# Kernel optimization log

Measured on AMD Instinct MI355X. Metric: run time of the kernel, lower is better.

Reference implementation:

```python
import jax, jax.numpy as jnp
import numpy as np

HEADS = 8
DQK = 64
DV = 64
SPAN = 32
STRIDE = 1


def setup_inputs() -> dict:
    key = jax.random.key(0)
    ks = jax.random.split(key, 7)
    B, Lq, Lkv = 2, 4096, 4096
    dq = dk = dv = 512
    dout = 512
    w_scale = 0.02
    return {
        "q": jax.random.normal(ks[0], (B, Lq, dq), jnp.float32),
        "k": jax.random.normal(ks[1], (B, Lkv, dk), jnp.float32),
        "v": jax.random.normal(ks[2], (B, Lkv, dv), jnp.float32),
        "Wq": jax.random.normal(ks[3], (dq, HEADS * DQK), jnp.float32) * w_scale,
        "Wk": jax.random.normal(ks[4], (dk, HEADS * DQK), jnp.float32) * w_scale,
        "Wv": jax.random.normal(ks[5], (dv, HEADS * DV), jnp.float32) * w_scale,
        "Wo": jax.random.normal(ks[6], (HEADS * DV, dout), jnp.float32) * w_scale,
    }


def reference(q, k, v, Wq, Wk, Wv, Wo):
    B, Lq, _ = q.shape
    Lkv = k.shape[1]
    # projections -> [B, H, L, d]
    Q = (q @ Wq).reshape(B, Lq, HEADS, DQK).transpose(0, 2, 1, 3)
    K = (k @ Wk).reshape(B, Lkv, HEADS, DQK).transpose(0, 2, 1, 3)
    V = (v @ Wv).reshape(B, Lkv, HEADS, DV).transpose(0, 2, 1, 3)

    # sliding window indices: kvi[r, j] = r - (span-1) + stride*j  -> [span, Lq]
    r = jnp.arange(SPAN)
    j = jnp.arange(Lq)
    kvi = r[:, None] - (SPAN - 1) + STRIDE * j[None, :]
    valid = (kvi >= 0) & (kvi < Lkv)                      # [span, Lq]
    kvs = jnp.clip(kvi, 0, Lkv - 1)

    Kg = K[:, :, kvs, :]                                   # [B, H, span, Lq, dQK]
    scores = jnp.einsum("bhjd,bhrjd->bhrj", Q, Kg) / (DQK ** 0.5)
    scores = jnp.where(valid, scores, -jnp.inf)
    # faithful to original: softmax over dim=3 == length_q axis
    W = jax.nn.softmax(scores, axis=3)                     # [B, H, span, Lq]
    W = jnp.where(valid, W, 0.0)

    Vg = V[:, :, kvs, :]                                   # [B, H, span, Lq, dV]
    O = jnp.einsum("bhrj,bhrjd->bhjd", W, Vg)              # sum over span
    out = O.transpose(0, 2, 1, 3).reshape(B, Lq, HEADS * DV) @ Wo
    return out
```

## Files before the change

kernel.cpp:

```cpp
#include <hip/hip_runtime.h>
#include <hip/hip_bf16.h>

#define L_Q 4096
#define NB 2
#define DMODEL 512
#define NHEAD 8
#define DHEAD 64
#define SPAN_ 32

using short8 = __attribute__((ext_vector_type(8))) short;
using f32x4  = __attribute__((ext_vector_type(4))) float;

typedef __attribute__((address_space(1))) const void GV;
typedef __attribute__((address_space(3))) void LV;

__device__ __forceinline__ void gl2lds16(const void* g, void* l) {
    __builtin_amdgcn_global_load_lds((GV*)g, (LV*)l, 16, 0, 0);
}

__device__ __forceinline__ float bf2f(short u) {
    return __uint_as_float(((unsigned)(unsigned short)u) << 16);
}
__device__ __forceinline__ short f2bf(float f) {
    __hip_bfloat16 h = __float2bfloat16(f);
    return *reinterpret_cast<short*>(&h);
}
__device__ __forceinline__ unsigned packbf(float lo, float hi) {
    return (unsigned)(unsigned short)f2bf(lo) | ((unsigned)(unsigned short)f2bf(hi) << 16);
}

__global__ __launch_bounds__(256) void castT4_bf16(
    const float* __restrict__ Wq, const float* __restrict__ Wk,
    const float* __restrict__ Wv, const float* __restrict__ Wo,
    short* __restrict__ Wtq, short* __restrict__ Wtk,
    short* __restrict__ Wtv, short* __restrict__ Wto)
{
    const int z = blockIdx.z;
    const float* W = (z == 0) ? Wq : ((z == 1) ? Wk : ((z == 2) ? Wv : Wo));
    short* Wt = (z == 0) ? Wtq : ((z == 1) ? Wtk : ((z == 2) ? Wtv : Wto));
    __shared__ float t[32][33];
    const int tx = threadIdx.x, ty = threadIdx.y;
    const int bx = blockIdx.x, by = blockIdx.y;
#pragma unroll
    for (int i = 0; i < 4; ++i)
        t[ty + i * 8][tx] = W[(size_t)(by * 32 + ty + i * 8) * DMODEL + bx * 32 + tx];
    __syncthreads();
#pragma unroll
    for (int i = 0; i < 4; ++i)
        Wt[(size_t)(bx * 32 + ty + i * 8) * DMODEL + by * 32 + tx] = f2bf(t[tx][ty + i * 8]);
}

__device__ __forceinline__ void xcd_swizzle(int& m0, int& n0) {
    int hw = blockIdx.x + (blockIdx.y << 2);
    int xcd = hw & 7, slot = hw >> 3;
    int mt = xcd * 8 + (slot >> 2);
    int nt = slot & 3;
    m0 = mt * 128;
    n0 = nt * 128;
}

template<int OUTMODE, bool AF32>
__device__ __forceinline__ void gemm128_body(
    const void* __restrict__ Avoid, const short* __restrict__ Bt, void* __restrict__ Cout,
    void* AsRaw, short* Bs, int m0, int n0)
{
    const int tid = threadIdx.x;
    const int w = tid >> 6, lane = tid & 63;
    const int wr = w & 1, wc = w >> 1;
    const int l15 = lane & 15, l4 = lane >> 4;
    float* Asf = (float*)AsRaw;
    short* Asb = (short*)AsRaw;

    f32x4 acc[4][4];
#pragma unroll
    for (int fm = 0; fm < 4; ++fm)
#pragma unroll
        for (int fn = 0; fn < 4; ++fn) acc[fm][fn] = (f32x4){0.f, 0.f, 0.f, 0.f};

    for (int k0 = 0; k0 < DMODEL; k0 += 64) {
        __syncthreads();
        if (AF32) {
            const float* Af = (const float*)Avoid;
#pragma unroll
            for (int it = 0; it < 8; ++it) {
                int c = it * 256 + tid;
                int row = c >> 4, slot = c & 15;
                gl2lds16(Af + (size_t)(m0 + row) * DMODEL + k0 + ((slot ^ (row & 15)) << 2),
                         &Asf[c * 4]);
            }
        } else {
            const short* Ab = (const short*)Avoid;
#pragma unroll
            for (int it = 0; it < 4; ++it) {
                int c = it * 256 + tid;
                int row = c >> 3, slot = c & 7;
                gl2lds16(Ab + (size_t)(m0 + row) * DMODEL + k0 + ((slot ^ (row & 7)) << 3),
                         &Asb[c * 8]);
            }
        }
#pragma unroll
        for (int it = 0; it < 4; ++it) {
            int c = it * 256 + tid;
            int row = c >> 3, slot = c & 7;
            gl2lds16(Bt + (size_t)(n0 + row) * DMODEL + k0 + ((slot ^ (row & 7)) << 3), &Bs[c * 8]);
        }
        __syncthreads();
#pragma unroll
        for (int ks = 0; ks < 2; ++ks) {
            const int koff = ks * 4 + l4;
            short8 a[4], b[4];
#pragma unroll
            for (int fm = 0; fm < 4; ++fm) {
                int row = wr * 64 + fm * 16 + l15;
                if (AF32) {
                    int rx = row & 15;
                    float4 f0 = *(const float4*)&Asf[row * 64 + (((koff * 2)     ^ rx) << 2)];
                    float4 f1 = *(const float4*)&Asf[row * 64 + (((koff * 2 + 1) ^ rx) << 2)];
                    short8 o;
                    o[0] = f2bf(f0.x); o[1] = f2bf(f0.y); o[2] = f2bf(f0.z); o[3] = f2bf(f0.w);
                    o[4] = f2bf(f1.x); o[5] = f2bf(f1.y); o[6] = f2bf(f1.z); o[7] = f2bf(f1.w);
                    a[fm] = o;
                } else {
                    a[fm] = *(const short8*)&Asb[(row * 8 + (koff ^ (row & 7))) * 8];
                }
            }
#pragma unroll
            for (int fn = 0; fn < 4; ++fn) {
                int row = wc * 64 + fn * 16 + l15;
                b[fn] = *(const short8*)&Bs[(row * 8 + (koff ^ (row & 7))) * 8];
            }
#pragma unroll
            for (int fm = 0; fm < 4; ++fm)
#pragma unroll
                for (int fn = 0; fn < 4; ++fn)
                    acc[fm][fn] = __builtin_amdgcn_mfma_f32_16x16x32_bf16(
                        a[fm], b[fn], acc[fm][fn], 0, 0, 0);
        }
    }
#pragma unroll
    for (int fm = 0; fm < 4; ++fm)
#pragma unroll
        for (int fn = 0; fn < 4; ++fn) {
            if (OUTMODE == 2) {
                short4 o4;
                o4.x = f2bf(acc[fm][fn][0]);
                o4.y = f2bf(acc[fm][fn][1]);
                o4.z = f2bf(acc[fm][fn][2]);
                o4.w = f2bf(acc[fm][fn][3]);
                int m = m0 + wr * 64 + fm * 16 + l4 * 4;
                int bb = m >> 12, g = m & (L_Q - 1);
                int n = n0 + wc * 64 + fn * 16 + l15;
                int hh = n >> 6, dd = n & 63;
                *(short4*)&((short*)Cout)[(((size_t)bb * NHEAD + hh) * DHEAD + dd) * L_Q + g] = o4;
            } else {
#pragma unroll
                for (int i = 0; i < 4; ++i) {
                    size_t row = (size_t)(m0 + wr * 64 + fm * 16 + l4 * 4 + i);
                    int col = n0 + wc * 64 + fn * 16 + l15;
                    if (OUTMODE == 1) ((short*)Cout)[row * DMODEL + col] = f2bf(acc[fm][fn][i]);
                    else              ((float*)Cout)[row * DMODEL + col] = acc[fm][fn][i];
                }
            }
        }
}

__global__ __launch_bounds__(256) void gemm_qkv(
    const float* __restrict__ q, const float* __restrict__ k, const float* __restrict__ v,
    const short* __restrict__ Wtq, const short* __restrict__ Wtk, const short* __restrict__ Wtv,
    short* __restrict__ Qp, short* __restrict__ Kp, short* __restrict__ Vt)
{
    __shared__ float Asf[128 * 64];
    __shared__ short Bs[128 * 64];
    int m0, n0;
    xcd_swizzle(m0, n0);
    const int z = blockIdx.z;
    const float* A  = (z == 0) ? q   : ((z == 1) ? k   : v);
    const short* Bt = (z == 0) ? Wtq : ((z == 1) ? Wtk : Wtv);
    if (z == 2) gemm128_body<2, true>(A, Bt, Vt, Asf, Bs, m0, n0);
    else        gemm128_body<1, true>(A, Bt, (z == 0) ? Qp : Kp, Asf, Bs, m0, n0);
}

__global__ __launch_bounds__(256) void gemm_fin(
    const short* __restrict__ Op, const short* __restrict__ Wto, float* __restrict__ out)
{
    __shared__ short As[128 * 64];
    __shared__ short Bs[128 * 64];
    int m0, n0;
    xcd_swizzle(m0, n0);
    gemm128_body<0, false>(Op, Wto, out, As, Bs, m0, n0);
}

__global__ __launch_bounds__(256) void attn_e(
    const short* __restrict__ Qp, const short* __restrict__ Kp,
    float* __restrict__ part)
{
    __shared__ short Ks[160 * 64];
    __shared__ short Qs[128 * 64];
    __shared__ float eb[128][36];
    __shared__ float red[8][32];
    const int tid = threadIdx.x;
    const int j0 = blockIdx.x * 128;
    const int h = blockIdx.y, b = blockIdx.z;
    const int bh = b * NHEAD + h;
    const int w = tid >> 6, lane = tid & 63;
    const int l15 = lane & 15, l4 = lane >> 4;

    {
        float4 z = make_float4(0.f, 0.f, 0.f, 0.f);
        float4* ebv = (float4*)&eb[0][0];
#pragma unroll
        for (int i = 0; i < 5; ++i) {
            int idx = i * 256 + tid;
            if (idx < 1152) ebv[idx] = z;
        }
    }
#pragma unroll
    for (int it = 0; it < 5; ++it) {
        int c = it * 256 + tid;
        int row = c >> 3, slot = c & 7;
        int g = j0 - 31 + row;
        g = (g < 0) ? 0 : ((g > L_Q - 1) ? L_Q - 1 : g);
        gl2lds16(Kp + ((size_t)b * L_Q + g) * DMODEL + h * DHEAD + ((slot ^ (row & 7)) << 3), &Ks[c * 8]);
    }
#pragma unroll
    for (int it = 0; it < 4; ++it) {
        int c = it * 256 + tid;
        int row = c >> 3, slot = c & 7;
        gl2lds16(Qp + ((size_t)b * L_Q + j0 + row) * DMODEL + h * DHEAD + ((slot ^ (row & 7)) << 3), &Qs[c * 8]);
    }
    __syncthreads();

    f32x4 acc[2][4];
#pragma unroll
    for (int tm = 0; tm < 2; ++tm)
#pragma unroll
        for (int tn = 0; tn < 4; ++tn) acc[tm][tn] = (f32x4){0.f, 0.f, 0.f, 0.f};
#pragma unroll
    for (int kk = 0; kk < 2; ++kk) {
        const int koff = kk * 4 + l4;
        short8 af[2], bf[4];
#pragma unroll
        for (int tm = 0; tm < 2; ++tm) {
            int row = w * 32 + tm * 16 + l15;
            af[tm] = *(const short8*)&Qs[(row * 8 + (koff ^ (row & 7))) * 8];
        }
#pragma unroll
        for (int tn = 0; tn < 4; ++tn) {
            int row = w * 32 + tn * 16 + l15;
            bf[tn] = *(const short8*)&Ks[(row * 8 + (koff ^ (row & 7))) * 8];
        }
#pragma unroll
        for (int tm = 0; tm < 2; ++tm)
#pragma unroll
            for (int tn = 0; tn < 4; ++tn)
                acc[tm][tn] = __builtin_amdgcn_mfma_f32_16x16x32_bf16(
                    af[tm], bf[tn], acc[tm][tn], 0, 0, 0);
    }

    const int gbase = j0 + w * 32 - 31;
#pragma unroll
    for (int tm = 0; tm < 2; ++tm)
#pragma unroll
        for (int tn = 0; tn < 4; ++tn)
#pragma unroll
            for (int i = 0; i < 4; ++i) {
                int q = tm * 16 + l4 * 4 + i;
                int rr = tn * 16 + l15;
                int r = rr - q;
                bool valid = (r >= 0) && (r < SPAN_) && (gbase + rr >= 0);
                if (valid) eb[w * 32 + q][r] = __expf(acc[tm][tn][i] * 0.125f);
            }
    __syncthreads();

    {
        int r = tid & 31, grp = tid >> 5;
        float s = 0.f;
#pragma unroll
        for (int qq = 0; qq < 16; ++qq) s += eb[grp * 16 + qq][r];
        red[grp][r] = s;
    }
    __syncthreads();
    if (tid < 32) {
        float s = 0.f;
#pragma unroll
        for (int g = 0; g < 8; ++g) s += red[g][tid];
        part[((size_t)bh * SPAN_ + tid) * 32 + blockIdx.x] = s;
    }
}

__global__ __launch_bounds__(256) void attn_o(
    const short* __restrict__ Qp, const short* __restrict__ Kp,
    const short* __restrict__ Vt, const float* __restrict__ part,
    short* __restrict__ Op)
{
    __shared__ short Ks[160 * 64];
    __shared__ short Qs[128 * 64];
    __shared__ short Vts[64 * 192];
    const int tid = threadIdx.x;
    const int j0 = blockIdx.x * 128;
    const int h = blockIdx.y, b = blockIdx.z;
    const int bh = b * NHEAD + h;
    const int w = tid >> 6, lane = tid & 63;
    const int l15 = lane & 15, l4 = lane >> 4;

#pragma unroll
    for (int it = 0; it < 5; ++it) {
        int c = it * 256 + tid;
        int row = c >> 3, slot = c & 7;
        int g = j0 - 32 + row;
        g = (g < 0) ? 0 : ((g > L_Q - 1) ? L_Q - 1 : g);
        gl2lds16(Kp + ((size_t)b * L_Q + g) * DMODEL + h * DHEAD + ((slot ^ (row & 7)) << 3), &Ks[c * 8]);
    }
#pragma unroll
    for (int it = 0; it < 4; ++it) {
        int c = it * 256 + tid;
        int row = c >> 3, slot = c & 7;
        gl2lds16(Qp + ((size_t)b * L_Q + j0 + row) * DMODEL + h * DHEAD + ((slot ^ (row & 7)) << 3), &Qs[c * 8]);
    }
#pragma unroll
    for (int it = 0; it < 6; ++it) {
        int c = it * 256 + tid;
        int d = c / 24, cs = c - d * 24;
        int gg = j0 - 32 + ((cs ^ (d & 7)) << 3);
        gg = (gg < 0) ? 0 : ((gg > L_Q - 8) ? L_Q - 8 : gg);
        gl2lds16(Vt + ((size_t)bh * DHEAD + d) * L_Q + gg, &Vts[c * 8]);
    }

    float iv;
    {
        const float4* pp = (const float4*)(part + ((size_t)bh * SPAN_ + (lane & 31)) * 32);
        float s = 0.f;
#pragma unroll
        for (int i = 0; i < 8; ++i) {
            float4 t = pp[i];
            s += t.x + t.y + t.z + t.w;
        }
        iv = 1.0f / s;
    }
    __syncthreads();

    f32x4 sa[4][2];
#pragma unroll
    for (int tk = 0; tk < 4; ++tk)
#pragma unroll
        for (int tq = 0; tq < 2; ++tq) sa[tk][tq] = (f32x4){0.f, 0.f, 0.f, 0.f};
#pragma unroll
    for (int kk = 0; kk < 2; ++kk) {
        const int koff = kk * 4 + l4;
        short8 af[4], qf[2];
#pragma unroll
        for (int tk = 0; tk < 4; ++tk) {
            int row = w * 32 + tk * 16 + l15;
            af[tk] = *(const short8*)&Ks[(row * 8 + (koff ^ (row & 7))) * 8];
        }
#pragma unroll
        for (int tq = 0; tq < 2; ++tq) {
            int row = w * 32 + tq * 16 + l15;
            qf[tq] = *(const short8*)&Qs[(row * 8 + (koff ^ (row & 7))) * 8];
        }
#pragma unroll
        for (int tk = 0; tk < 4; ++tk)
#pragma unroll
            for (int tq = 0; tq < 2; ++tq)
                sa[tk][tq] = __builtin_amdgcn_mfma_f32_16x16x32_bf16(
                    af[tk], qf[tq], sa[tk][tq], 0, 0, 0);
    }

    const int gbase = j0 + w * 32 - 32;
#pragma unroll
    for (int tk = 0; tk < 4; ++tk)
#pragma unroll
        for (int tq = 0; tq < 2; ++tq)
#pragma unroll
            for (int i = 0; i < 4; ++i) {
                int rrp = tk * 16 + l4 * 4 + i;
                int q = tq * 16 + l15;
                int r = rrp - q - 1;
                bool valid = (r >= 0) && (r < SPAN_) && (gbase + rrp >= 0);
                float e = __expf(sa[tk][tq][i] * 0.125f) * __shfl(iv, r & 31);
                sa[tk][tq][i] = valid ? e : 0.f;
            }

    unsigned pk[4][2][2];
#pragma unroll
    for (int tk = 0; tk < 4; ++tk)
#pragma unroll
        for (int tq = 0; tq < 2; ++tq) {
            pk[tk][tq][0] = packbf(sa[tk][tq][0], sa[tk][tq][1]);
            pk[tk][tq][1] = packbf(sa[tk][tq][2], sa[tk][tq][3]);
        }

    const int hi = l4 >> 1;
    const int lsA = ((l4 & 1) << 5) + l15;

    f32x4 oa[2][4];
#pragma unroll
    for (int tm = 0; tm < 2; ++tm)
#pragma unroll
        for (int dn = 0; dn < 4; ++dn) oa[tm][dn] = (f32x4){0.f, 0.f, 0.f, 0.f};
#pragma unroll
    for (int kk = 0; kk < 2; ++kk) {
        short8 pa[2];
#pragma unroll
        for (int tm = 0; tm < 2; ++tm) {
            unsigned lo00 = (unsigned)__shfl((int)pk[kk * 2 + 0][tm][0], lsA);
            unsigned hi00 = (unsigned)__shfl((int)pk[kk * 2 + 1][tm][0], lsA);
            unsigned lo01 = (unsigned)__shfl((int)pk[kk * 2 + 0][tm][1], lsA);
            unsigned hi01 = (unsigned)__shfl((int)pk[kk * 2 + 1][tm][1], lsA);
            unsigned lo10 = (unsigned)__shfl((int)pk[kk * 2 + 0][tm][0], lsA + 16);
            unsigned hi10 = (unsigned)__shfl((int)pk[kk * 2 + 1][tm][0], lsA + 16);
            unsigned lo11 = (unsigned)__shfl((int)pk[kk * 2 + 0][tm][1], lsA + 16);
            unsigned hi11 = (unsigned)__shfl((int)pk[kk * 2 + 1][tm][1], lsA + 16);
            uint4 wds;
            wds.x = hi ? hi00 : lo00;
            wds.y = hi ? hi01 : lo01;
            wds.z = hi ? hi10 : lo10;
            wds.w = hi ? hi11 : lo11;
            pa[tm] = *reinterpret_cast<short8*>(&wds);
        }
#pragma unroll
        for (int dn = 0; dn < 4; ++dn) {
            int row = dn * 16 + l15;
            int cs = w * 4 + kk * 4 + l4;
            short8 vb = *(const short8*)&Vts[row * 192 + ((cs ^ (row & 7)) << 3)];
#pragma unroll
            for (int tm = 0; tm < 2; ++tm)
                oa[tm][dn] = __builtin_amdgcn_mfma_f32_16x16x32_bf16(
                    pa[tm], vb, oa[tm][dn], 0, 0, 0);
        }
    }

#pragma unroll
    for (int tm = 0; tm < 2; ++tm)
#pragma unroll
        for (int dn = 0; dn < 4; ++dn)
#pragma unroll
            for (int i = 0; i < 4; ++i) {
                int q = w * 32 + tm * 16 + l4 * 4 + i;
                Op[((size_t)b * L_Q + j0 + q) * DMODEL + h * DHEAD + dn * 16 + l15] =
                    f2bf(oa[tm][dn][i]);
            }
}

extern "C" void kernel_launch(void* const* d_in, const int* in_sizes, int n_in,
                              void* d_out, int out_size, void* d_ws, size_t ws_size,
                              hipStream_t stream) {
    (void)in_sizes; (void)n_in; (void)out_size; (void)ws_size;
    const float* q  = (const float*)d_in[0];
    const float* k  = (const float*)d_in[1];
    const float* v  = (const float*)d_in[2];
    const float* Wq = (const float*)d_in[3];
    const float* Wk = (const float*)d_in[4];
    const float* Wv = (const float*)d_in[5];
    const float* Wo = (const float*)d_in[6];
    float* out = (float*)d_out;

    char* ws = (char*)d_ws;
    const size_t MiB = 1ull << 20;
    short* Wtq = (short*)(ws);
    short* Wtk = (short*)(ws + 512 * 1024);
    short* Wtv = (short*)(ws + 1 * MiB);
    short* Wto = (short*)(ws + 1 * MiB + 512 * 1024);
    short* Qp  = (short*)(ws + 2 * MiB);
    short* Kp  = (short*)(ws + 10 * MiB);
    short* Vtp = (short*)(ws + 18 * MiB);
    short* Op  = (short*)(ws + 26 * MiB);
    float* part = (float*)(ws + 34 * MiB);

    castT4_bf16<<<dim3(16, 16, 4), dim3(32, 8), 0, stream>>>(
        Wq, Wk, Wv, Wo, Wtq, Wtk, Wtv, Wto);

    gemm_qkv<<<dim3(4, 64, 3), 256, 0, stream>>>(q, k, v, Wtq, Wtk, Wtv, Qp, Kp, Vtp);

    dim3 ga(L_Q / 128, NHEAD, NB);
    attn_e<<<ga, 256, 0, stream>>>(Qp, Kp, part);
    attn_o<<<ga, 256, 0, stream>>>(Qp, Kp, Vtp, part, Op);

    gemm_fin<<<dim3(4, 64), 256, 0, stream>>>(Op, Wto, out);
}
```

Before: 64.18 us.

## Double-buffer GEMM LDS tiles and merge QKV projections into one persistent loop

The two projection GEMMs now double-buffer their LDS tiles, prefetching the next K-slice with global_load_lds while MFMAs run on the current one, with a single barrier per step. The QKV kernel no longer launches a z-dimension; each block loops over all three projections in sequence (24 stages), writing each output after 8 stages and resetting its accumulators. The aim is to hide global load latency and cut barriers. In exchange the QKV grid shrinks to 256 blocks, and QKV LDS use doubles to about 96KB, which can lower occupancy.

```diff
diff --git a/kernel.cpp b/kernel.cpp
--- a/kernel.cpp
+++ b/kernel.cpp
@@ -59,135 +59,193 @@
     n0 = nt * 128;
 }
 
-template<int OUTMODE, bool AF32>
-__device__ __forceinline__ void gemm128_body(
-    const void* __restrict__ Avoid, const short* __restrict__ Bt, void* __restrict__ Cout,
-    void* AsRaw, short* Bs, int m0, int n0)
-{
-    const int tid = threadIdx.x;
-    const int w = tid >> 6, lane = tid & 63;
-    const int wr = w & 1, wc = w >> 1;
-    const int l15 = lane & 15, l4 = lane >> 4;
-    float* Asf = (float*)AsRaw;
-    short* Asb = (short*)AsRaw;
-
-    f32x4 acc[4][4];
-#pragma unroll
-    for (int fm = 0; fm < 4; ++fm)
-#pragma unroll
-        for (int fn = 0; fn < 4; ++fn) acc[fm][fn] = (f32x4){0.f, 0.f, 0.f, 0.f};
-
-    for (int k0 = 0; k0 < DMODEL; k0 += 64) {
-        __syncthreads();
-        if (AF32) {
-            const float* Af = (const float*)Avoid;
-#pragma unroll
-            for (int it = 0; it < 8; ++it) {
-                int c = it * 256 + tid;
-                int row = c >> 4, slot = c & 15;
-                gl2lds16(Af + (size_t)(m0 + row) * DMODEL + k0 + ((slot ^ (row & 15)) << 2),
-                         &Asf[c * 4]);
-            }
-        } else {
-            const short* Ab = (const short*)Avoid;
-#pragma unroll
-            for (int it = 0; it < 4; ++it) {
-                int c = it * 256 + tid;
-                int row = c >> 3, slot = c & 7;
-                gl2lds16(Ab + (size_t)(m0 + row) * DMODEL + k0 + ((slot ^ (row & 7)) << 3),
-                         &Asb[c * 8]);
-            }
-        }
-#pragma unroll
-        for (int it = 0; it < 4; ++it) {
-            int c = it * 256 + tid;
-            int row = c >> 3, slot = c & 7;
-            gl2lds16(Bt + (size_t)(n0 + row) * DMODEL + k0 + ((slot ^ (row & 7)) << 3), &Bs[c * 8]);
-        }
-        __syncthreads();
-#pragma unroll
-        for (int ks = 0; ks < 2; ++ks) {
-            const int koff = ks * 4 + l4;
-            short8 a[4], b[4];
-#pragma unroll
-            for (int fm = 0; fm < 4; ++fm) {
-                int row = wr * 64 + fm * 16 + l15;
-                if (AF32) {
-                    int rx = row & 15;
-                    float4 f0 = *(const float4*)&Asf[row * 64 + (((koff * 2)     ^ rx) << 2)];
-                    float4 f1 = *(const float4*)&Asf[row * 64 + (((koff * 2 + 1) ^ rx) << 2)];
-                    short8 o;
-                    o[0] = f2bf(f0.x); o[1] = f2bf(f0.y); o[2] = f2bf(f0.z); o[3] = f2bf(f0.w);
-                    o[4] = f2bf(f1.x); o[5] = f2bf(f1.y); o[6] = f2bf(f1.z); o[7] = f2bf(f1.w);
-                    a[fm] = o;
-                } else {
-                    a[fm] = *(const short8*)&Asb[(row * 8 + (koff ^ (row & 7))) * 8];
-                }
-            }
-#pragma unroll
-            for (int fn = 0; fn < 4; ++fn) {
-                int row = wc * 64 + fn * 16 + l15;
-                b[fn] = *(const short8*)&Bs[(row * 8 + (koff ^ (row & 7))) * 8];
-            }
-#pragma unroll
-            for (int fm = 0; fm < 4; ++fm)
-#pragma unroll
-                for (int fn = 0; fn < 4; ++fn)
-                    acc[fm][fn] = __builtin_amdgcn_mfma_f32_16x16x32_bf16(
-                        a[fm], b[fn], acc[fm][fn], 0, 0, 0);
-        }
-    }
-#pragma unroll
-    for (int fm = 0; fm < 4; ++fm)
-#pragma unroll
-        for (int fn = 0; fn < 4; ++fn) {
-            if (OUTMODE == 2) {
-                short4 o4;
-                o4.x = f2bf(acc[fm][fn][0]);
-                o4.y = f2bf(acc[fm][fn][1]);
-                o4.z = f2bf(acc[fm][fn][2]);
-                o4.w = f2bf(acc[fm][fn][3]);
-                int m = m0 + wr * 64 + fm * 16 + l4 * 4;
-                int bb = m >> 12, g = m & (L_Q - 1);
-                int n = n0 + wc * 64 + fn * 16 + l15;
-                int hh = n >> 6, dd = n & 63;
-                *(short4*)&((short*)Cout)[(((size_t)bb * NHEAD + hh) * DHEAD + dd) * L_Q + g] = o4;
-            } else {
-#pragma unroll
-                for (int i = 0; i < 4; ++i) {
-                    size_t row = (size_t)(m0 + wr * 64 + fm * 16 + l4 * 4 + i);
-                    int col = n0 + wc * 64 + fn * 16 + l15;
-                    if (OUTMODE == 1) ((short*)Cout)[row * DMODEL + col] = f2bf(acc[fm][fn][i]);
-                    else              ((float*)Cout)[row * DMODEL + col] = acc[fm][fn][i];
-                }
-            }
-        }
-}
-
 __global__ __launch_bounds__(256) void gemm_qkv(
     const float* __restrict__ q, const float* __restrict__ k, const float* __restrict__ v,
     const short* __restrict__ Wtq, const short* __restrict__ Wtk, const short* __restrict__ Wtv,
     short* __restrict__ Qp, short* __restrict__ Kp, short* __restrict__ Vt)
 {
-    __shared__ float Asf[128 * 64];
-    __shared__ short Bs[128 * 64];
+    __shared__ float AsF[2][128 * 64];
+    __shared__ short Bs[2][128 * 64];
     int m0, n0;
     xcd_swizzle(m0, n0);
-    const int z = blockIdx.z;
-    const float* A  = (z == 0) ? q   : ((z == 1) ? k   : v);
-    const short* Bt = (z == 0) ? Wtq : ((z == 1) ? Wtk : Wtv);
-    if (z == 2) gemm128_body<2, true>(A, Bt, Vt, Asf, Bs, m0, n0);
-    else        gemm128_body<1, true>(A, Bt, (z == 0) ? Qp : Kp, Asf, Bs, m0, n0);
+    const int tid = threadIdx.x;
+    const int w = tid >> 6, lane = tid & 63;
+    const int wr = w & 1, wc = w >> 1;
+    const int l15 = lane & 15, l4 = lane >> 4;
+
+    auto stage = [&](int idx, int buf) {
+        const int z = idx >> 3;
+        const int k0 = (idx & 7) << 6;
+        const float* Af = (z == 0) ? q : ((z == 1) ? k : v);
+        const short* Bt = (z == 0) ? Wtq : ((z == 1) ? Wtk : Wtv);
+#pragma unroll
+        for (int it = 0; it < 8; ++it) {
+            int c = it * 256 + tid;
+            int row = c >> 4, slot = c & 15;
+            gl2lds16(Af + (size_t)(m0 + row) * DMODEL + k0 + ((slot ^ (row & 15)) << 2),
+                     &AsF[buf][c * 4]);
+        }
+#pragma unroll
+        for (int it = 0; it < 4; ++it) {
+            int c = it * 256 + tid;
+            int row = c >> 3, slot = c & 7;
+            gl2lds16(Bt + (size_t)(n0 + row) * DMODEL + k0 + ((slot ^ (row & 7)) << 3),
+                     &Bs[buf][c * 8]);
+        }
+    };
+
+    f32x4 acc[4][4];
+#pragma unroll
+    for (int fm = 0; fm < 4; ++fm)
+#pragma unroll
+        for (int fn = 0; fn < 4; ++fn) acc[fm][fn] = (f32x4){0.f, 0.f, 0.f, 0.f};
+
+    stage(0, 0);
+    __syncthreads();
+    int cur = 0;
+
+    for (int idx = 0; idx < 24; ++idx) {
+        if (idx < 23) stage(idx + 1, cur ^ 1);
+
+#pragma unroll
+        for (int ks = 0; ks < 2; ++ks) {
+            const int koff = ks * 4 + l4;
+            short8 a[4], b[4];
+#pragma unroll
+            for (int fm = 0; fm < 4; ++fm) {
+                int row = wr * 64 + fm * 16 + l15;
+                int rx = row & 15;
+                float4 f0 = *(const float4*)&AsF[cur][row * 64 + (((koff * 2)     ^ rx) << 2)];
+                float4 f1 = *(const float4*)&AsF[cur][row * 64 + (((koff * 2 + 1) ^ rx) << 2)];
+                short8 o;
+                o[0] = f2bf(f0.x); o[1] = f2bf(f0.y); o[2] = f2bf(f0.z); o[3] = f2bf(f0.w);
+                o[4] = f2bf(f1.x); o[5] = f2bf(f1.y); o[6] = f2bf(f1.z); o[7] = f2bf(f1.w);
+                a[fm] = o;
+            }
+#pragma unroll
+            for (int fn = 0; fn < 4; ++fn) {
+                int row = wc * 64 + fn * 16 + l15;
+                b[fn] = *(const short8*)&Bs[cur][(row * 8 + (koff ^ (row & 7))) * 8];
+            }
+#pragma unroll
+            for (int fm = 0; fm < 4; ++fm)
+#pragma unroll
+                for (int fn = 0; fn < 4; ++fn)
+                    acc[fm][fn] = __builtin_amdgcn_mfma_f32_16x16x32_bf16(
+                        a[fm], b[fn], acc[fm][fn], 0, 0, 0);
+        }
+
+        if ((idx & 7) == 7) {
+            const int z = idx >> 3;
+            short* OutB = (z == 0) ? Qp : Kp;
+#pragma unroll
+            for (int fm = 0; fm < 4; ++fm)
+#pragma unroll
+                for (int fn = 0; fn < 4; ++fn) {
+                    if (z == 2) {
+                        short4 o4;
+                        o4.x = f2bf(acc[fm][fn][0]);
+                        o4.y = f2bf(acc[fm][fn][1]);
+                        o4.z = f2bf(acc[fm][fn][2]);
+                        o4.w = f2bf(acc[fm][fn][3]);
+                        int m = m0 + wr * 64 + fm * 16 + l4 * 4;
+                        int bb = m >> 12, g = m & (L_Q - 1);
+                        int n = n0 + wc * 64 + fn * 16 + l15;
+                        int hh = n >> 6, dd = n & 63;
+                        *(short4*)&Vt[(((size_t)bb * NHEAD + hh) * DHEAD + dd) * L_Q + g] = o4;
+                    } else {
+#pragma unroll
+                        for (int i = 0; i < 4; ++i) {
+                            size_t row = (size_t)(m0 + wr * 64 + fm * 16 + l4 * 4 + i);
+                            int col = n0 + wc * 64 + fn * 16 + l15;
+                            OutB[row * DMODEL + col] = f2bf(acc[fm][fn][i]);
+                        }
+                    }
+                    acc[fm][fn] = (f32x4){0.f, 0.f, 0.f, 0.f};
+                }
+        }
+        __syncthreads();
+        cur ^= 1;
+    }
 }
 
 __global__ __launch_bounds__(256) void gemm_fin(
     const short* __restrict__ Op, const short* __restrict__ Wto, float* __restrict__ out)
 {
-    __shared__ short As[128 * 64];
-    __shared__ short Bs[128 * 64];
+    __shared__ short As[2][128 * 64];
+    __shared__ short Bs[2][128 * 64];
     int m0, n0;
     xcd_swizzle(m0, n0);
-    gemm128_body<0, false>(Op, Wto, out, As, Bs, m0, n0);
+    const int tid = threadIdx.x;
+    const int w = tid >> 6, lane = tid & 63;
+    const int wr = w & 1, wc = w >> 1;
+    const int l15 = lane & 15, l4 = lane >> 4;
+
+    auto stage = [&](int t, int buf) {
+        const int k0 = t << 6;
+#pragma unroll
+        for (int it = 0; it < 4; ++it) {
+            int c = it * 256 + tid;
+            int row = c >> 3, slot = c & 7;
+            gl2lds16(Op + (size_t)(m0 + row) * DMODEL + k0 + ((slot ^ (row & 7)) << 3),
+                     &As[buf][c * 8]);
+        }
+#pragma unroll
+        for (int it = 0; it < 4; ++it) {
+            int c = it * 256 + tid;
+            int row = c >> 3, slot = c & 7;
+            gl2lds16(Wto + (size_t)(n0 + row) * DMODEL + k0 + ((slot ^ (row & 7)) << 3),
+                     &Bs[buf][c * 8]);
+        }
+    };
+
+    f32x4 acc[4][4];
+#pragma unroll
+    for (int fm = 0; fm < 4; ++fm)
+#pragma unroll
+        for (int fn = 0; fn < 4; ++fn) acc[fm][fn] = (f32x4){0.f, 0.f, 0.f, 0.f};
+
+    stage(0, 0);
+    __syncthreads();
+    int cur = 0;
+
+    for (int t = 0; t < 8; ++t) {
+        if (t < 7) stage(t + 1, cur ^ 1);
+#pragma unroll
+        for (int ks = 0; ks < 2; ++ks) {
+            const int koff = ks * 4 + l4;
+            short8 a[4], b[4];
+#pragma unroll
+            for (int fm = 0; fm < 4; ++fm) {
+                int row = wr * 64 + fm * 16 + l15;
+                a[fm] = *(const short8*)&As[cur][(row * 8 + (koff ^ (row & 7))) * 8];
+            }
+#pragma unroll
+            for (int fn = 0; fn < 4; ++fn) {
+                int row = wc * 64 + fn * 16 + l15;
+                b[fn] = *(const short8*)&Bs[cur][(row * 8 + (koff ^ (row & 7))) * 8];
+            }
+#pragma unroll
+            for (int fm = 0; fm < 4; ++fm)
+#pragma unroll
+                for (int fn = 0; fn < 4; ++fn)
+                    acc[fm][fn] = __builtin_amdgcn_mfma_f32_16x16x32_bf16(
+                        a[fm], b[fn], acc[fm][fn], 0, 0, 0);
+        }
+        __syncthreads();
+        cur ^= 1;
+    }
+
+#pragma unroll
+    for (int fm = 0; fm < 4; ++fm)
+#pragma unroll
+        for (int fn = 0; fn < 4; ++fn)
+#pragma unroll
+            for (int i = 0; i < 4; ++i) {
+                size_t row = (size_t)(m0 + wr * 64 + fm * 16 + l4 * 4 + i);
+                int col = n0 + wc * 64 + fn * 16 + l15;
+                out[row * DMODEL + col] = acc[fm][fn][i];
+            }
 }
 
 __global__ __launch_bounds__(256) void attn_e(
@@ -470,7 +528,7 @@
     castT4_bf16<<<dim3(16, 16, 4), dim3(32, 8), 0, stream>>>(
         Wq, Wk, Wv, Wo, Wtq, Wtk, Wtv, Wto);
 
-    gemm_qkv<<<dim3(4, 64, 3), 256, 0, stream>>>(q, k, v, Wtq, Wtk, Wtv, Qp, Kp, Vtp);
+    gemm_qkv<<<dim3(4, 64), 256, 0, stream>>>(q, k, v, Wtq, Wtk, Wtv, Qp, Kp, Vtp);
 
     dim3 ga(L_Q / 128, NHEAD, NB);
     attn_e<<<ga, 256, 0, stream>>>(Qp, Kp, part);
```

After: 93.33 us. 1.45x slower.
